# Optimization experiments

Measured on AMD Instinct MI355X. Metric: run time of the kernel, lower is better.

Reference implementation:

```python
import jax, jax.numpy as jnp
import numpy as np
from jax import lax

EPS = 1e-5

def gelu(x):
    return jax.nn.gelu(x, approximate=False)  # torch nn.GELU default (erf)

def conv1d(x, w, b):
    # x: (N, Cin, L), w: (Cout, Cin, K), SAME padding, stride 1
    y = lax.conv_general_dilated(x, w, window_strides=(1,), padding='SAME',
                                 dimension_numbers=('NCH', 'OIH', 'NCH'))
    return y + b[None, :, None]

def setup_inputs() -> dict:
    key = jax.random.key(0)
    ks = jax.random.split(key, 16)
    B, C, P, L, D = 8, 129, 62, 20, 256
    s = lambda k, shape, fan: jax.random.normal(k, shape, jnp.float32) * (1.0 / np.sqrt(fan))
    return {
        'x': jax.random.normal(ks[0], (B, C, P, L), jnp.float32),
        'conv1_w': s(ks[1], (64, 1, 3), 3),   'conv1_b': jnp.zeros((64,), jnp.float32),
        'conv2_w': s(ks[2], (128, 64, 3), 192), 'conv2_b': jnp.zeros((128,), jnp.float32),
        'conv3_w': s(ks[3], (D, 128, 3), 384),  'conv3_b': jnp.zeros((D,), jnp.float32),
        'mix_w': s(ks[4], (C, C), C), 'mix_b': jnp.zeros((C,), jnp.float32),
        'ln_w': jnp.ones((C,), jnp.float32), 'ln_b': jnp.zeros((C,), jnp.float32),
        'proj_w': s(ks[5], (D, D), D), 'proj_b': jnp.zeros((D,), jnp.float32),
    }

def reference(x, conv1_w, conv1_b, conv2_w, conv2_b, conv3_w, conv3_b,
              mix_w, mix_b, ln_w, ln_b, proj_w, proj_b):
    B, C, P, L = x.shape
    D = conv3_w.shape[0]
    # temporal conv stack over flattened (B*C*P, 1, L)
    h = x.reshape(B * C * P, 1, L)
    h = gelu(conv1d(h, conv1_w, conv1_b))
    h = gelu(conv1d(h, conv2_w, conv2_b))
    N, Ch, Lh = h.shape
    h = h.reshape(N, Ch, Lh // 2, 2).max(axis=-1)  # MaxPool1d(2)
    h = gelu(conv1d(h, conv3_w, conv3_b))
    feat = h.mean(axis=-1)                                  # (B*C*P, D)
    feat = feat.reshape(B, C, P, D).transpose(0, 2, 1, 3)   # (B, P, C, D)
    t = feat.reshape(B * P, C, D).transpose(0, 2, 1)        # (B*P, D, C) == per-feature slices
    # channel_mix: Linear(C,C) + GELU + LayerNorm(C), vectorized over the dim axis
    m = gelu(jnp.einsum('ndc,oc->ndo', t, mix_w) + mix_b)
    mu = m.mean(axis=-1, keepdims=True)
    var = ((m - mu) ** 2).mean(axis=-1, keepdims=True)
    m = (m - mu) * lax.rsqrt(var + EPS) * ln_w + ln_b
    mixed = m.transpose(0, 2, 1).reshape(B, P, C, D)
    out = jnp.einsum('bpcd,ed->bpce', mixed, proj_w) + proj_b
    return out.transpose(0, 2, 1, 3)                        # (B, C, P, D)
```

## Files before the change

kernel.cpp:

```cpp
#include <hip/hip_runtime.h>

#define B_ 8
#define C_ 129
#define P_ 62
#define L_ 20
#define D_ 256
#define NSEG (B_*C_*P_)
#define N2   (B_*P_)
#define SEGB 16
#define NWG  (NSEG/SEGB)

#define S1 1416
#define S2 1544

#define FT_STRIDE 168
#define MT_STRIDE 264

typedef short short8 __attribute__((ext_vector_type(8)));
typedef float f32x4  __attribute__((ext_vector_type(4)));

__device__ __forceinline__ float gelu_f(float x) {
    float u  = 0.70710678f * x;
    float au = __builtin_fabsf(u);
    float t  = __builtin_amdgcn_rcpf(fmaf(0.3275911f, au, 1.0f));
    float p  = fmaf(1.061405429f, t, -1.453152027f);
    p = fmaf(p, t, 1.421413741f);
    p = fmaf(p, t, -0.284496736f);
    p = fmaf(p, t, 0.254829592f);
    p = p * t;
    float e  = __builtin_amdgcn_exp2f(-1.4426950409f * au * au);
    float ea = fmaf(-p, e, 1.0f);
    float er = copysignf(ea, u);
    return 0.5f * x * (1.0f + er);
}
__device__ __forceinline__ unsigned short f2bf(float f) {
    unsigned u = __float_as_uint(f);
    u = u + 0x7FFFu + ((u >> 16) & 1u);
    return (unsigned short)(u >> 16);
}

__global__ void prep_kernel(const float* __restrict__ w2, const float* __restrict__ w3,
                            const float* __restrict__ mw, const float* __restrict__ pw,
                            const float* __restrict__ mixb, const float* __restrict__ lnw,
                            const float* __restrict__ lnb,
                            unsigned short* __restrict__ A2p, unsigned short* __restrict__ A3p,
                            unsigned short* __restrict__ mixA, unsigned short* __restrict__ projA,
                            float* __restrict__ bmixp, float* __restrict__ lnwp,
                            float* __restrict__ lnbp) {
    int idx = blockIdx.x * blockDim.x + threadIdx.x;
    int stride = gridDim.x * blockDim.x;
    for (int f = idx; f < 6*8*64*8; f += stride) {
        int j = f & 7, ln = (f >> 3) & 63, mt = (f >> 9) & 7, kt = f >> 12;
        int co = mt*16 + (ln & 15);
        int k  = kt >> 1;
        int ci = (kt & 1)*32 + (ln >> 4)*8 + j;
        A2p[f] = f2bf(w2[(co*64 + ci)*3 + k]);
    }
    for (int f = idx; f < 12*16*64*8; f += stride) {
        int j = f & 7, ln = (f >> 3) & 63, mt = (f >> 9) & 15, kt = f >> 13;
        int co = mt*16 + (ln & 15);
        int k  = kt >> 2;
        int ci = (kt & 3)*32 + (ln >> 4)*8 + j;
        A3p[f] = f2bf(w3[(co*128 + ci)*3 + k]);
    }
    for (int f = idx; f < 5*9*64*8; f += stride) {
        int j = f & 7, ln = (f >> 3) & 63;
        int mt = (f >> 9) % 9, kt = (f >> 9) / 9;
        int o = mt*16 + (ln & 15);
        int c = kt*32 + (ln >> 4)*8 + j;
        mixA[f] = (o < 129 && c < 129) ? f2bf(mw[o*129 + c]) : (unsigned short)0;
    }
    for (int f = idx; f < 8*16*64*8; f += stride) {
        int j = f & 7, ln = (f >> 3) & 63, mt = (f >> 9) & 15, kt = f >> 13;
        int e = mt*16 + (ln & 15);
        int d = kt*32 + (ln >> 4)*8 + j;
        projA[f] = f2bf(pw[e*256 + d]);
    }
    for (int i = idx; i < 144; i += stride) {
        bmixp[i] = (i < 129) ? mixb[i] : 0.f;
        lnwp[i]  = (i < 129) ? lnw[i]  : 0.f;
        lnbp[i]  = (i < 129) ? lnb[i]  : 0.f;
    }
}

__global__ __launch_bounds__(512, 2) void conv_mfma_kernel(
    const float* __restrict__ x,
    const float* __restrict__ w1, const float* __restrict__ b1,
    const unsigned short* __restrict__ A2p, const float* __restrict__ b2,
    const unsigned short* __restrict__ A3p, const float* __restrict__ b3,
    float* __restrict__ feat)
{
    __shared__ __align__(16) unsigned short h1T[SEGB * S1];
    __shared__ __align__(16) unsigned short hpT[SEGB * S2];
    __shared__ float xs[SEGB][22];

    const int t = threadIdx.x;
    const int wave = t >> 6, lane = t & 63;
    const int sL = lane & 15, gL = lane >> 4;
    const int seg0 = blockIdx.x * SEGB;

    for (int idx = t; idx < SEGB*22; idx += 512) {
        int s = idx / 22, i = idx % 22;
        float v = 0.f;
        if (i >= 1 && i <= 20) v = x[(seg0 + s)*L_ + i - 1];
        xs[s][i] = v;
    }
    for (int idx = t; idx < SEGB*64; idx += 512) {
        int s = idx >> 6, ci = idx & 63;
        h1T[s*S1 + ci] = 0;
        h1T[s*S1 + 21*64 + ci] = 0;
    }
    for (int idx = t; idx < SEGB*128; idx += 512) {
        int s = idx >> 7, co = idx & 127;
        hpT[s*S2 + co] = 0;
        hpT[s*S2 + 11*128 + co] = 0;
    }
    __syncthreads();

    {
        int seg = t >> 5, cp = t & 31;
        int ci0 = cp * 2;
        float wa0 = w1[ci0*3+0], wa1 = w1[ci0*3+1], wa2 = w1[ci0*3+2], ba = b1[ci0];
        float wb0 = w1[ci0*3+3], wb1 = w1[ci0*3+4], wb2 = w1[ci0*3+5], bb = b1[ci0+1];
        unsigned short* dst = &h1T[seg*S1 + ci0];
        #pragma unroll
        for (int l = 0; l < 20; ++l) {
            float x0 = xs[seg][l], x1 = xs[seg][l+1], x2v = xs[seg][l+2];
            float va = fmaf(x0, wa0, fmaf(x1, wa1, fmaf(x2v, wa2, ba)));
            float vb = fmaf(x0, wb0, fmaf(x1, wb1, fmaf(x2v, wb2, bb)));
            unsigned pk = (unsigned)f2bf(gelu_f(va)) | ((unsigned)f2bf(gelu_f(vb)) << 16);
            *(unsigned*)(dst + (l+1)*64) = pk;
        }
    }
    __syncthreads();

    {
        const int mh = wave & 3, ng = wave >> 2;
        f32x4 acc[2][10];
        #pragma unroll
        for (int mi = 0; mi < 2; ++mi)
            #pragma unroll
            for (int li = 0; li < 10; ++li) acc[mi][li] = (f32x4){0.f,0.f,0.f,0.f};

        const unsigned short* h1base = &h1T[sL*S1 + ng*640 + gL*8];
        #pragma unroll
        for (int h = 0; h < 2; ++h) {
            short8 br[12];
            #pragma unroll
            for (int r = 0; r < 12; ++r)
                br[r] = *(const short8*)(h1base + r*64 + h*32);
            #pragma unroll
            for (int k = 0; k < 3; ++k) {
                int kt = k*2 + h;
                short8 a0 = *(const short8*)(A2p + (((kt*8 + mh*2 + 0)*64 + lane) << 3));
                short8 a1 = *(const short8*)(A2p + (((kt*8 + mh*2 + 1)*64 + lane) << 3));
                #pragma unroll
                for (int li = 0; li < 10; ++li) {
                    acc[0][li] = __builtin_amdgcn_mfma_f32_16x16x32_bf16(a0, br[li+k], acc[0][li], 0, 0, 0);
                    acc[1][li] = __builtin_amdgcn_mfma_f32_16x16x32_bf16(a1, br[li+k], acc[1][li], 0, 0, 0);
                }
            }
        }
        #pragma unroll
        for (int mi = 0; mi < 2; ++mi) {
            int mt = mh*2 + mi;
            int co0 = mt*16 + gL*4;
            float4 bb = *(const float4*)(b2 + co0);
            float bbr[4] = {bb.x, bb.y, bb.z, bb.w};
            #pragma unroll
            for (int j = 0; j < 5; ++j) {
                int lp = ng*5 + j;
                unsigned short pk[4];
                #pragma unroll
                for (int r = 0; r < 4; ++r) {
                    float p0 = gelu_f(acc[mi][2*j][r]   + bbr[r]);
                    float p1 = gelu_f(acc[mi][2*j+1][r] + bbr[r]);
                    pk[r] = f2bf(fmaxf(p0, p1));
                }
                *(uint2*)&hpT[sL*S2 + (lp+1)*128 + co0] = *(uint2*)pk;
            }
        }
    }
    __syncthreads();

    {
        f32x4 acc[2][10];
        #pragma unroll
        for (int mi = 0; mi < 2; ++mi)
            #pragma unroll
            for (int li = 0; li < 10; ++li) acc[mi][li] = (f32x4){0.f,0.f,0.f,0.f};

        const unsigned short* hpbase = &hpT[sL*S2 + gL*8];
        #pragma unroll
        for (int q = 0; q < 4; ++q) {
            short8 br[12];
            #pragma unroll
            for (int r = 0; r < 12; ++r)
                br[r] = *(const short8*)(hpbase + r*128 + q*32);
            #pragma unroll
            for (int k = 0; k < 3; ++k) {
                int kt = k*4 + q;
                short8 a0 = *(const short8*)(A3p + (((kt*16 + wave*2 + 0)*64 + lane) << 3));
                short8 a1 = *(const short8*)(A3p + (((kt*16 + wave*2 + 1)*64 + lane) << 3));
                #pragma unroll
                for (int li = 0; li < 10; ++li) {
                    acc[0][li] = __builtin_amdgcn_mfma_f32_16x16x32_bf16(a0, br[li+k], acc[0][li], 0, 0, 0);
                    acc[1][li] = __builtin_amdgcn_mfma_f32_16x16x32_bf16(a1, br[li+k], acc[1][li], 0, 0, 0);
                }
            }
        }
        int seg = seg0 + sL;
        int bI = seg / (C_*P_);
        int rem = seg % (C_*P_);
        int c = rem / P_, p = rem % P_;
        float* frow = feat + (((size_t)(bI*P_ + p)*C_ + c) << 8);
        #pragma unroll
        for (int mi = 0; mi < 2; ++mi) {
            int co0 = (wave*2 + mi)*16 + gL*4;
            float4 bv = *(const float4*)(b3 + co0);
            float bbr[4] = {bv.x, bv.y, bv.z, bv.w};
            float sum[4] = {0.f, 0.f, 0.f, 0.f};
            #pragma unroll
            for (int li = 0; li < 10; ++li)
                #pragma unroll
                for (int r = 0; r < 4; ++r)
                    sum[r] += gelu_f(acc[mi][li][r] + bbr[r]);
            float4 o;
            o.x = sum[0]*0.1f; o.y = sum[1]*0.1f; o.z = sum[2]*0.1f; o.w = sum[3]*0.1f;
            *(float4*)(frow + co0) = o;
        }
    }
}

__global__ __launch_bounds__(512, 2) void mix_proj_kernel(
    const float* __restrict__ feat,
    const unsigned short* __restrict__ mixA, const float* __restrict__ bmixp,
    const float* __restrict__ lnwp, const float* __restrict__ lnbp,
    const unsigned short* __restrict__ projA, const float* __restrict__ proj_b,
    float* __restrict__ out)
{
    __shared__ __align__(16) unsigned short ulds[256*FT_STRIDE];
    unsigned short* fT = ulds;
    unsigned short* mT = ulds;

    const int t = threadIdx.x;
    const int wave = t >> 6, lane = t & 63;
    const int sL = lane & 15, gL = lane >> 4;
    const int n2 = blockIdx.x;
    const int b = n2 / P_, p = n2 % P_;

    const float* fbase = feat + (size_t)n2 * C_ * 256;
    for (int idx = t; idx < 129*256; idx += 512) {
        int c = idx >> 8, d = idx & 255;
        fT[d*FT_STRIDE + c] = f2bf(fbase[idx]);
    }
    for (int idx = t; idx < 256*31; idx += 512) {
        int d = idx / 31, c = 129 + idx % 31;
        fT[d*FT_STRIDE + c] = 0;
    }
    __syncthreads();

    f32x4 acc[9][2];
    #pragma unroll
    for (int mt = 0; mt < 9; ++mt)
        #pragma unroll
        for (int nt = 0; nt < 2; ++nt) acc[mt][nt] = (f32x4){0.f,0.f,0.f,0.f};

    #pragma unroll
    for (int kt = 0; kt < 5; ++kt) {
        short8 bb[2];
        #pragma unroll
        for (int nt = 0; nt < 2; ++nt) {
            int d = (wave*2 + nt)*16 + sL;
            bb[nt] = *(const short8*)&fT[d*FT_STRIDE + kt*32 + gL*8];
        }
        #pragma unroll
        for (int mt = 0; mt < 9; ++mt) {
            short8 a = *(const short8*)(mixA + (((kt*9 + mt)*64 + lane) << 3));
            #pragma unroll
            for (int nt = 0; nt < 2; ++nt)
                acc[mt][nt] = __builtin_amdgcn_mfma_f32_16x16x32_bf16(a, bb[nt], acc[mt][nt], 0, 0, 0);
        }
    }

    float sum[2] = {0.f, 0.f}, sq[2] = {0.f, 0.f};
    #pragma unroll
    for (int mt = 0; mt < 9; ++mt) {
        float4 bv = *(const float4*)(bmixp + mt*16 + gL*4);
        float bbr[4] = {bv.x, bv.y, bv.z, bv.w};
        #pragma unroll
        for (int nt = 0; nt < 2; ++nt) {
            #pragma unroll
            for (int r = 0; r < 4; ++r) {
                int o = mt*16 + gL*4 + r;
                float g = (o < 129) ? gelu_f(acc[mt][nt][r] + bbr[r]) : 0.f;
                acc[mt][nt][r] = g;
                sum[nt] += g;
                sq[nt]  += g*g;
            }
        }
    }
    float mu[2], rs[2];
    #pragma unroll
    for (int nt = 0; nt < 2; ++nt) {
        float s = sum[nt], q = sq[nt];
        s += __shfl_xor(s, 16); q += __shfl_xor(q, 16);
        s += __shfl_xor(s, 32); q += __shfl_xor(q, 32);
        mu[nt] = s * (1.f/129.f);
        float var = q * (1.f/129.f) - mu[nt]*mu[nt];
        rs[nt] = rsqrtf(var + 1e-5f);
    }

    __syncthreads();

    #pragma unroll
    for (int mt = 0; mt < 9; ++mt) {
        float4 lw = *(const float4*)(lnwp + mt*16 + gL*4);
        float4 lb = *(const float4*)(lnbp + mt*16 + gL*4);
        float lwr[4] = {lw.x, lw.y, lw.z, lw.w};
        float lbr[4] = {lb.x, lb.y, lb.z, lb.w};
        #pragma unroll
        for (int nt = 0; nt < 2; ++nt) {
            int d = (wave*2 + nt)*16 + sL;
            #pragma unroll
            for (int r = 0; r < 4; ++r) {
                int o = mt*16 + gL*4 + r;
                float y = (acc[mt][nt][r] - mu[nt]) * rs[nt] * lwr[r] + lbr[r];
                mT[o*MT_STRIDE + d] = f2bf(y);
            }
        }
    }
    __syncthreads();

    f32x4 pacc[2][9];
    #pragma unroll
    for (int mi = 0; mi < 2; ++mi)
        #pragma unroll
        for (int nt = 0; nt < 9; ++nt) pacc[mi][nt] = (f32x4){0.f,0.f,0.f,0.f};

    #pragma unroll
    for (int kt = 0; kt < 8; ++kt) {
        short8 a[2];
        #pragma unroll
        for (int mi = 0; mi < 2; ++mi)
            a[mi] = *(const short8*)(projA + (((kt*16 + wave*2 + mi)*64 + lane) << 3));
        #pragma unroll
        for (int nt = 0; nt < 9; ++nt) {
            short8 bb = *(const short8*)&mT[(nt*16 + sL)*MT_STRIDE + kt*32 + gL*8];
            #pragma unroll
            for (int mi = 0; mi < 2; ++mi)
                pacc[mi][nt] = __builtin_amdgcn_mfma_f32_16x16x32_bf16(a[mi], bb, pacc[mi][nt], 0, 0, 0);
        }
    }

    #pragma unroll
    for (int mi = 0; mi < 2; ++mi) {
        int e0 = (wave*2 + mi)*16 + gL*4;
        float4 pb4 = *(const float4*)(proj_b + e0);
        #pragma unroll
        for (int nt = 0; nt < 9; ++nt) {
            int c = nt*16 + sL;
            if (c < 129) {
                float4 o4;
                o4.x = pacc[mi][nt][0] + pb4.x;
                o4.y = pacc[mi][nt][1] + pb4.y;
                o4.z = pacc[mi][nt][2] + pb4.z;
                o4.w = pacc[mi][nt][3] + pb4.w;
                *(float4*)&out[(((size_t)(b*C_ + c)*P_) + p)*256 + e0] = o4;
            }
        }
    }
}

extern "C" void kernel_launch(void* const* d_in, const int* in_sizes, int n_in,
                              void* d_out, int out_size, void* d_ws, size_t ws_size,
                              hipStream_t stream) {
    (void)in_sizes; (void)n_in; (void)out_size; (void)ws_size;
    const float* x    = (const float*)d_in[0];
    const float* w1   = (const float*)d_in[1];
    const float* b1   = (const float*)d_in[2];
    const float* w2   = (const float*)d_in[3];
    const float* b2   = (const float*)d_in[4];
    const float* w3   = (const float*)d_in[5];
    const float* b3   = (const float*)d_in[6];
    const float* mixw = (const float*)d_in[7];
    const float* mixb = (const float*)d_in[8];
    const float* lnw  = (const float*)d_in[9];
    const float* lnb  = (const float*)d_in[10];
    const float* pw   = (const float*)d_in[11];
    const float* pb   = (const float*)d_in[12];
    float* out = (float*)d_out;
    float* ws  = (float*)d_ws;

    float* feat = ws;
    unsigned short* A2p  = (unsigned short*)(ws + 16379904);
    unsigned short* A3p  = A2p + 24576;
    unsigned short* mixA = A3p + 98304;
    unsigned short* projA = mixA + 23040;
    float* bmixp = (float*)(projA + 65536);
    float* lnwp  = bmixp + 144;
    float* lnbp  = lnwp + 144;

    prep_kernel<<<256, 256, 0, stream>>>(w2, w3, mixw, pw, mixb, lnw, lnb,
                                         A2p, A3p, mixA, projA, bmixp, lnwp, lnbp);
    conv_mfma_kernel<<<NWG, 512, 0, stream>>>(x, w1, b1, A2p, b2, A3p, b3, feat);
    mix_proj_kernel<<<N2, 512, 0, stream>>>(feat, mixA, bmixp, lnwp, lnbp, projA, pb, out);
}
```

Before: 390.9 us.

## Halve segments per block and split positions across lanes to raise occupancy

Each workgroup now handles 8 segments instead of 16, and the 16 MFMA B-rows are remapped as 8 segments × 2 position halves. The maxpool and the mean are finished with cross-lane shuffles, and only half the lanes write results. Accumulator and B-register arrays are halved, so launch bounds ask for 4 blocks per CU instead of 2, which should hide latency better. In exchange the kernel adds shuffles and idle lanes on stores, and the weight A fragments are reloaded twice as often per segment.

Result: no change. 388.5 us (-0.6%).

```diff
diff --git a/kernel.cpp b/kernel.cpp
--- a/kernel.cpp
+++ b/kernel.cpp
@@ -7,7 +7,7 @@
 #define D_ 256
 #define NSEG (B_*C_*P_)
 #define N2   (B_*P_)
-#define SEGB 16
+#define SEGB 8
 #define NWG  (NSEG/SEGB)
 
 #define S1 1416
@@ -83,7 +83,7 @@
     }
 }
 
-__global__ __launch_bounds__(512, 2) void conv_mfma_kernel(
+__global__ __launch_bounds__(512, 4) void conv_mfma_kernel(
     const float* __restrict__ x,
     const float* __restrict__ w1, const float* __restrict__ b1,
     const unsigned short* __restrict__ A2p, const float* __restrict__ b2,
@@ -97,6 +97,7 @@
     const int t = threadIdx.x;
     const int wave = t >> 6, lane = t & 63;
     const int sL = lane & 15, gL = lane >> 4;
+    const int seg8 = sL & 7, hi8 = sL >> 3;
     const int seg0 = blockIdx.x * SEGB;
 
     for (int idx = t; idx < SEGB*22; idx += 512) {
@@ -118,13 +119,15 @@
     __syncthreads();
 
     {
-        int seg = t >> 5, cp = t & 31;
+        int seg = wave;
+        int cp = (lane >> 1) & 31, ph = lane & 1;
         int ci0 = cp * 2;
         float wa0 = w1[ci0*3+0], wa1 = w1[ci0*3+1], wa2 = w1[ci0*3+2], ba = b1[ci0];
         float wb0 = w1[ci0*3+3], wb1 = w1[ci0*3+4], wb2 = w1[ci0*3+5], bb = b1[ci0+1];
         unsigned short* dst = &h1T[seg*S1 + ci0];
         #pragma unroll
-        for (int l = 0; l < 20; ++l) {
+        for (int i = 0; i < 10; ++i) {
+            int l = ph*10 + i;
             float x0 = xs[seg][l], x1 = xs[seg][l+1], x2v = xs[seg][l+2];
             float va = fmaf(x0, wa0, fmaf(x1, wa1, fmaf(x2v, wa2, ba)));
             float vb = fmaf(x0, wb0, fmaf(x1, wb1, fmaf(x2v, wb2, bb)));
@@ -136,18 +139,18 @@
 
     {
         const int mh = wave & 3, ng = wave >> 2;
-        f32x4 acc[2][10];
+        f32x4 acc[2][5];
         #pragma unroll
         for (int mi = 0; mi < 2; ++mi)
             #pragma unroll
-            for (int li = 0; li < 10; ++li) acc[mi][li] = (f32x4){0.f,0.f,0.f,0.f};
-
-        const unsigned short* h1base = &h1T[sL*S1 + ng*640 + gL*8];
+            for (int n = 0; n < 5; ++n) acc[mi][n] = (f32x4){0.f,0.f,0.f,0.f};
+
+        const unsigned short* h1base = &h1T[seg8*S1 + (ng*10 + hi8)*64 + gL*8];
         #pragma unroll
         for (int h = 0; h < 2; ++h) {
-            short8 br[12];
-            #pragma unroll
-            for (int r = 0; r < 12; ++r)
+            short8 br[11];
+            #pragma unroll
+            for (int r = 0; r < 11; ++r)
                 br[r] = *(const short8*)(h1base + r*64 + h*32);
             #pragma unroll
             for (int k = 0; k < 3; ++k) {
@@ -155,9 +158,9 @@
                 short8 a0 = *(const short8*)(A2p + (((kt*8 + mh*2 + 0)*64 + lane) << 3));
                 short8 a1 = *(const short8*)(A2p + (((kt*8 + mh*2 + 1)*64 + lane) << 3));
                 #pragma unroll
-                for (int li = 0; li < 10; ++li) {
-                    acc[0][li] = __builtin_amdgcn_mfma_f32_16x16x32_bf16(a0, br[li+k], acc[0][li], 0, 0, 0);
-                    acc[1][li] = __builtin_amdgcn_mfma_f32_16x16x32_bf16(a1, br[li+k], acc[1][li], 0, 0, 0);
+                for (int n = 0; n < 5; ++n) {
+                    acc[0][n] = __builtin_amdgcn_mfma_f32_16x16x32_bf16(a0, br[2*n+k], acc[0][n], 0, 0, 0);
+                    acc[1][n] = __builtin_amdgcn_mfma_f32_16x16x32_bf16(a1, br[2*n+k], acc[1][n], 0, 0, 0);
                 }
             }
         }
@@ -168,34 +171,38 @@
             float4 bb = *(const float4*)(b2 + co0);
             float bbr[4] = {bb.x, bb.y, bb.z, bb.w};
             #pragma unroll
-            for (int j = 0; j < 5; ++j) {
-                int lp = ng*5 + j;
-                unsigned short pk[4];
+            for (int n = 0; n < 5; ++n) {
+                int lp = ng*5 + n;
+                float pv[4];
                 #pragma unroll
                 for (int r = 0; r < 4; ++r) {
-                    float p0 = gelu_f(acc[mi][2*j][r]   + bbr[r]);
-                    float p1 = gelu_f(acc[mi][2*j+1][r] + bbr[r]);
-                    pk[r] = f2bf(fmaxf(p0, p1));
+                    float g = gelu_f(acc[mi][n][r] + bbr[r]);
+                    pv[r] = fmaxf(g, __shfl_xor(g, 8));
                 }
-                *(uint2*)&hpT[sL*S2 + (lp+1)*128 + co0] = *(uint2*)pk;
+                if (hi8 == 0) {
+                    unsigned short pk[4];
+                    #pragma unroll
+                    for (int r = 0; r < 4; ++r) pk[r] = f2bf(pv[r]);
+                    *(uint2*)&hpT[seg8*S2 + (lp+1)*128 + co0] = *(uint2*)pk;
+                }
             }
         }
     }
     __syncthreads();
 
     {
-        f32x4 acc[2][10];
+        f32x4 acc[2][5];
         #pragma unroll
         for (int mi = 0; mi < 2; ++mi)
             #pragma unroll
-            for (int li = 0; li < 10; ++li) acc[mi][li] = (f32x4){0.f,0.f,0.f,0.f};
-
-        const unsigned short* hpbase = &hpT[sL*S2 + gL*8];
+            for (int n = 0; n < 5; ++n) acc[mi][n] = (f32x4){0.f,0.f,0.f,0.f};
+
+        const unsigned short* hpbase = &hpT[seg8*S2 + hi8*128 + gL*8];
         #pragma unroll
         for (int q = 0; q < 4; ++q) {
-            short8 br[12];
-            #pragma unroll
-            for (int r = 0; r < 12; ++r)
+            short8 br[11];
+            #pragma unroll
+            for (int r = 0; r < 11; ++r)
                 br[r] = *(const short8*)(hpbase + r*128 + q*32);
             #pragma unroll
             for (int k = 0; k < 3; ++k) {
@@ -203,13 +210,13 @@
                 short8 a0 = *(const short8*)(A3p + (((kt*16 + wave*2 + 0)*64 + lane) << 3));
                 short8 a1 = *(const short8*)(A3p + (((kt*16 + wave*2 + 1)*64 + lane) << 3));
                 #pragma unroll
-                for (int li = 0; li < 10; ++li) {
-                    acc[0][li] = __builtin_amdgcn_mfma_f32_16x16x32_bf16(a0, br[li+k], acc[0][li], 0, 0, 0);
-                    acc[1][li] = __builtin_amdgcn_mfma_f32_16x16x32_bf16(a1, br[li+k], acc[1][li], 0, 0, 0);
+                for (int n = 0; n < 5; ++n) {
+                    acc[0][n] = __builtin_amdgcn_mfma_f32_16x16x32_bf16(a0, br[2*n+k], acc[0][n], 0, 0, 0);
+                    acc[1][n] = __builtin_amdgcn_mfma_f32_16x16x32_bf16(a1, br[2*n+k], acc[1][n], 0, 0, 0);
                 }
             }
         }
-        int seg = seg0 + sL;
+        int seg = seg0 + seg8;
         int bI = seg / (C_*P_);
         int rem = seg % (C_*P_);
         int c = rem / P_, p = rem % P_;
@@ -221,13 +228,18 @@
             float bbr[4] = {bv.x, bv.y, bv.z, bv.w};
             float sum[4] = {0.f, 0.f, 0.f, 0.f};
             #pragma unroll
-            for (int li = 0; li < 10; ++li)
+            for (int n = 0; n < 5; ++n)
                 #pragma unroll
                 for (int r = 0; r < 4; ++r)
-                    sum[r] += gelu_f(acc[mi][li][r] + bbr[r]);
-            float4 o;
-            o.x = sum[0]*0.1f; o.y = sum[1]*0.1f; o.z = sum[2]*0.1f; o.w = sum[3]*0.1f;
-            *(float4*)(frow + co0) = o;
+                    sum[r] += gelu_f(acc[mi][n][r] + bbr[r]);
+            #pragma unroll
+            for (int r = 0; r < 4; ++r)
+                sum[r] += __shfl_xor(sum[r], 8);
+            if (hi8 == 0) {
+                float4 o;
+                o.x = sum[0]*0.1f; o.y = sum[1]*0.1f; o.z = sum[2]*0.1f; o.w = sum[3]*0.1f;
+                *(float4*)(frow + co0) = o;
+            }
         }
     }
 }
```
